# Performance work log

Hardware: AMD Instinct MI355X
Metric: run time of the kernel (lower is better)

The kernel has to match this reference:

```python
import jax, jax.numpy as jnp
import numpy as np

N, E, DIN, HID, G, L = 50000, 200000, 128, 128, 64, 6
H1, H2 = 8, 4
EPS_LN, EPS_BN = 1e-5, 1e-5


def setup_inputs() -> dict:
    key = jax.random.key(0)
    ks = iter(jax.random.split(key, 32))
    def nrm(shape, scale=0.05):
        return jax.random.normal(next(ks), shape, dtype=jnp.float32) * scale
    z = lambda *s: jnp.zeros(s, jnp.float32)
    o = lambda *s: jnp.ones(s, jnp.float32)
    return {
        'x': jax.random.normal(next(ks), (N, DIN), dtype=jnp.float32),
        'edge_index': jax.random.randint(next(ks), (2, E), 0, N),
        'batch': jnp.sort(jax.random.randint(next(ks), (N,), 0, G)),
        'W1': nrm((DIN, H1 * HID)), 'a_src1': nrm((H1, HID)), 'a_dst1': nrm((H1, HID)), 'b1': z(H1 * HID),
        'W2': nrm((H1 * HID, H2 * HID)), 'a_src2': nrm((H2, HID)), 'a_dst2': nrm((H2, HID)), 'b2': z(H2 * HID),
        'W3': nrm((H2 * HID, HID)), 'b3': z(HID),
        'wq': nrm((L, HID, HID)), 'bq': z(L, HID), 'wk': nrm((L, HID, HID)), 'bk': z(L, HID),
        'wv': nrm((L, HID, HID)), 'bv': z(L, HID), 'wo': nrm((L, HID, HID)), 'bo': z(L, HID),
        'ln1g': o(L, HID), 'ln1b': z(L, HID), 'ln2g': o(L, HID), 'ln2b': z(L, HID),
        'wf1': nrm((L, HID, 4 * HID)), 'bf1': z(L, 4 * HID), 'wf2': nrm((L, 4 * HID, HID)), 'bf2': z(L, HID),
        'bn1_g': o(2 * HID), 'bn1_b': z(2 * HID),
        'fc1_w': nrm((2 * HID, HID // 2)), 'fc1_b': z(HID // 2),
        'bn2_g': o(HID // 2), 'bn2_b': z(HID // 2),
        'fc2_w': nrm((HID // 2, 2)), 'fc2_b': z(2),
    }


def _ln(x, g, b):
    mu = x.mean(-1, keepdims=True)
    v = ((x - mu) ** 2).mean(-1, keepdims=True)
    return (x - mu) * jax.lax.rsqrt(v + EPS_LN) * g + b


def _gat(x, src, dst, W, a_s, a_d, b, heads):
    # PyG GATConv: message src -> dst, segment softmax over incoming edges per dst.
    h = (x @ W).reshape(x.shape[0], heads, -1)           # [N, H, C]
    e = jax.nn.leaky_relu((h * a_s).sum(-1)[src] + (h * a_d).sum(-1)[dst], 0.2)  # [E, H]
    m = jax.ops.segment_max(e, dst, num_segments=N)
    ex = jnp.exp(e - jnp.where(jnp.isfinite(m), m, 0.0)[dst])
    s = jax.ops.segment_sum(ex, dst, num_segments=N)
    alpha = ex / (s[dst] + 1e-16)
    out = jax.ops.segment_sum(alpha[:, :, None] * h[src], dst, num_segments=N)
    return out.reshape(N, -1) + b


def _forward(x, edge_index, batch, W1, a_src1, a_dst1, b1, W2, a_src2, a_dst2, b2, W3, b3,
             wq, bq, wk, bk, wv, bv, wo, bo, ln1g, ln1b, ln2g, ln2b, wf1, bf1, wf2, bf2,
             bn1_g, bn1_b, fc1_w, fc1_b, bn2_g, bn2_b, fc2_w, fc2_b):
    loop = jnp.arange(N, dtype=edge_index.dtype)
    src = jnp.concatenate([edge_index[0], loop])          # add self-loops (PyG default)
    dst = jnp.concatenate([edge_index[1], loop])
    h = jax.nn.elu(_gat(x, src, dst, W1, a_src1, a_dst1, b1, H1))
    h = jax.nn.elu(_gat(h, src, dst, W2, a_src2, a_dst2, b2, H2))
    # GCNConv with symmetric normalization (self-loops already included)
    deg = jax.ops.segment_sum(jnp.ones(src.shape, h.dtype), dst, num_segments=N)
    dinv = jnp.where(deg > 0, jax.lax.rsqrt(jnp.maximum(deg, 1e-12)), 0.0)
    norm = dinv[src] * dinv[dst]
    h = jax.nn.elu(jax.ops.segment_sum(norm[:, None] * (h @ W3)[src], dst, num_segments=N) + b3)
    # TransformerEncoder over seq_len=1 (h3.unsqueeze(1)): softmax over one key == 1,
    # so MHA output == Wo @ (Wv h + bv) + bo exactly; q/k have no effect on the output.
    for l in range(L):
        sa = (h @ wv[l] + bv[l]) @ wo[l] + bo[l]
        h = _ln(h + sa, ln1g[l], ln1b[l])
        ff = jax.nn.gelu(h @ wf1[l] + bf1[l], approximate=False) @ wf2[l] + bf2[l]
        h = _ln(h + ff, ln2g[l], ln2b[l])
    # global mean / max pool over graphs
    cnt = jax.ops.segment_sum(jnp.ones((N,), h.dtype), batch, num_segments=G)
    hm = jax.ops.segment_sum(h, batch, num_segments=G) / jnp.maximum(cnt, 1.0)[:, None]
    hx = jax.ops.segment_max(h, batch, num_segments=G)
    hx = jnp.where(jnp.isfinite(hx), hx, 0.0)
    hc = jnp.concatenate([hm, hx], axis=1)                # [G, 2*HID]
    bn_s = 1.0 / np.sqrt(1.0 + EPS_BN)                    # eval BN: running stats (0, 1)
    hc = hc * bn_s * bn1_g + bn1_b
    hc = jax.nn.elu(hc @ fc1_w + fc1_b)
    hc = hc * bn_s * bn2_g + bn2_b
    return hc @ fc2_w + fc2_b                             # [G, 2]


def reference(x, edge_index, batch, W1, a_src1, a_dst1, b1, W2, a_src2, a_dst2, b2, W3, b3,
              wq, bq, wk, bk, wv, bv, wo, bo, ln1g, ln1b, ln2g, ln2b, wf1, bf1, wf2, bf2,
              bn1_g, bn1_b, fc1_w, fc1_b, bn2_g, bn2_b, fc2_w, fc2_b):
    return _forward(x, edge_index, batch, W1, a_src1, a_dst1, b1, W2, a_src2, a_dst2, b2, W3, b3,
                    wq, bq, wk, bk, wv, bv, wo, bo, ln1g, ln1b, ln2g, ln2b, wf1, bf1, wf2, bf2,
                    bn1_g, bn1_b, fc1_w, fc1_b, bn2_g, bn2_b, fc2_w, fc2_b)
```

## Files before the change

kernel.cpp:

```cpp
#include <hip/hip_runtime.h>
#include <hip/hip_bf16.h>
#include <math.h>

#define NN 50000
#define EE 200000
#define ET 250000
#define GG 64
#define LL 6

using short8 = __attribute__((ext_vector_type(8))) short;
using f32x4  = __attribute__((ext_vector_type(4))) float;
typedef unsigned short ushortT;

__device__ __forceinline__ float elu1(float x) { return x > 0.f ? x : expm1f(x); }
__device__ __forceinline__ float gelu_exact(float x) {
    return 0.5f * x * (1.f + erff(x * 0.70710678118654752440f));
}
__device__ __forceinline__ short f2bf(float f) {
    __hip_bfloat16 h = __float2bfloat16(f);
    return *reinterpret_cast<short*>(&h);
}
__device__ __forceinline__ float bf2f(ushortT u) {
    return __uint_as_float(((unsigned)u) << 16);
}

__global__ void count_deg_kernel(const int* __restrict__ ei, int* __restrict__ deg) {
    int e = blockIdx.x * 256 + threadIdx.x;
    if (e >= ET) return;
    int dst = (e < EE) ? ei[EE + e] : (e - EE);
    atomicAdd(&deg[dst], 1);
}

__global__ void scan_kernel(const int* __restrict__ deg, int* __restrict__ row_ptr, int n) {
    __shared__ int s[1024];
    int tid = threadIdx.x;
    const int per = (n + 1023) / 1024;
    int lo = tid * per, hi = min(lo + per, n);
    int sum = 0;
    for (int i = lo; i < hi; i++) sum += deg[i];
    s[tid] = sum;
    __syncthreads();
    for (int off = 1; off < 1024; off <<= 1) {
        int t = (tid >= off) ? s[tid - off] : 0;
        __syncthreads();
        s[tid] += t;
        __syncthreads();
    }
    int run = s[tid] - sum;
    for (int i = lo; i < hi; i++) { row_ptr[i] = run; run += deg[i]; }
    if (tid == 1023) row_ptr[n] = s[1023];
}

__global__ void fill_csr_kernel(const int* __restrict__ ei, const int* __restrict__ row_ptr,
                                int* __restrict__ cursor, int* __restrict__ edge_src) {
    int e = blockIdx.x * 256 + threadIdx.x;
    if (e >= ET) return;
    int src, dst;
    if (e < EE) { src = ei[e]; dst = ei[EE + e]; }
    else        { src = e - EE; dst = e - EE; }
    int pos = atomicAdd(&cursor[dst], 1);
    edge_src[row_ptr[dst] + pos] = src;
}

__global__ void dinv_kernel(const int* __restrict__ row_ptr, float* __restrict__ dinv) {
    int n = blockIdx.x * 256 + threadIdx.x;
    if (n >= NN) return;
    int d = row_ptr[n + 1] - row_ptr[n];
    dinv[n] = (d > 0) ? rsqrtf((float)d) : 0.f;
}

__global__ void wvwo_kernel(const float* __restrict__ wv, const float* __restrict__ wo,
                            const float* __restrict__ bv, const float* __restrict__ bo,
                            float* __restrict__ Wvo, float* __restrict__ bvo) {
    int l = blockIdx.y;
    const float* Wv = wv + l * 16384;
    const float* Wo = wo + l * 16384;
    int tid = blockIdx.x * 256 + threadIdx.x;
    if (tid < 16384) {
        int r = tid >> 7, c = tid & 127;
        float s = 0.f;
        for (int k = 0; k < 128; k++) s += Wv[r * 128 + k] * Wo[k * 128 + c];
        Wvo[l * 16384 + tid] = s;
    }
    if (blockIdx.x == 0 && threadIdx.x < 128) {
        int c = threadIdx.x;
        float s = bo[l * 128 + c];
        for (int k = 0; k < 128; k++) s += bv[l * 128 + k] * Wo[k * 128 + c];
        bvo[l * 128 + c] = s;
    }
}

__global__ void bprep_kernel(const float* __restrict__ B, short* __restrict__ Bp,
                             int K, int N, int ldb, long srcStride) {
    int layer = blockIdx.y;
    const float* Bsrc = B + srcStride * layer;
    short* Bd = Bp + (size_t)K * N * layer;
    int total = (K >> 5) * (N >> 4) * 64;
    int tid = blockIdx.x * 256 + threadIdx.x;
    if (tid >= total) return;
    int l = tid & 63;
    int rest = tid >> 6;
    int kbc = K >> 5;
    int kb = rest % kbc;
    int c16 = rest / kbc;
    int n = c16 * 16 + (l & 15);
    int kbase = kb * 32 + (l >> 4) * 8;
    short v[8];
#pragma unroll
    for (int j = 0; j < 8; j++) v[j] = f2bf(Bsrc[(size_t)(kbase + j) * ldb + n]);
    *(uint4*)(Bd + (size_t)tid * 8) = *(uint4*)v;
}

__global__ void cast_bf16_kernel(const float* __restrict__ in, short* __restrict__ out, int n4) {
    int i = blockIdx.x * 256 + threadIdx.x;
    if (i >= n4) return;
    float4 v = *(const float4*)(in + (size_t)i * 4);
    short s[4] = { f2bf(v.x), f2bf(v.y), f2bf(v.z), f2bf(v.w) };
    *(uint2*)(out + (size_t)i * 4) = *(uint2*)s;
}

template <int EPI, bool BIAS, bool OUTBF16, int NSPLIT, int KBC>
__global__ __launch_bounds__(256) void gemm_bf16_kernel(
    const short* __restrict__ A, const short* __restrict__ Bp,
    const float* __restrict__ bias, void* __restrict__ Cv,
    const float* __restrict__ a_s, const float* __restrict__ a_d,
    float* __restrict__ as_out, float* __restrict__ ad_out, int asH,
    const ushortT* __restrict__ Rres, const float* __restrict__ lng,
    const float* __restrict__ lnb, float* __restrict__ Qout,
    __hip_bfloat16* __restrict__ Qbout,
    int M, int K, int Nc) {
    __shared__ short Bs[(KBC > 0) ? KBC * 4096 : 8192];
    int t = threadIdx.x;
    int w = t >> 6, l = t & 63;
    int ln = l & 15, lq = l >> 4;
    int MBceil = (M + 63) >> 6;
    int bx = blockIdx.x;
    int xcd = bx & 7, idx = bx >> 3;
    int t2 = idx % NSPLIT;
    int mb = (idx / NSPLIT) * 8 + xcd;
    if (mb >= MBceil) return;
    int bm = mb * 64 + w * 16;
    int arow = bm + ln;
    bool aok = arow < M;
    int rowb = bm + lq * 4;
    const short* Ap = A + (size_t)arow * K + lq * 8;

    f32x4 acc[8];
#pragma unroll
    for (int j = 0; j < 8; j++) acc[j] = (f32x4){0.f, 0.f, 0.f, 0.f};

    if constexpr (KBC > 0) {
        {
            const uint4* src = (const uint4*)(Bp + (size_t)t2 * KBC * 4096);
            uint4* dst = (uint4*)Bs;
#pragma unroll
            for (int i = 0; i < KBC * 2; i++)
                dst[i * 256 + t] = src[i * 256 + t];
        }
        short8 af[KBC];
#pragma unroll
        for (int kb = 0; kb < KBC; kb++)
            af[kb] = aok ? *(const short8*)(Ap + kb * 32) : (short8){0,0,0,0,0,0,0,0};
        __syncthreads();
#pragma unroll
        for (int kb = 0; kb < KBC; kb++)
#pragma unroll
            for (int ct = 0; ct < 8; ct++) {
                short8 bfr = *(const short8*)(Bs + ((ct * KBC + kb) * 64 + l) * 8);
                acc[ct] = __builtin_amdgcn_mfma_f32_16x16x32_bf16(af[kb], bfr, acc[ct], 0, 0, 0);
            }
    } else {
        int kbc = K >> 5;
        int sct = t >> 5, spart = t & 31;
        auto stage = [&](int buf, int kb) {
            const uint4* src = (const uint4*)(Bp + ((size_t)(t2 * 8 + sct) * kbc + kb) * 512);
            uint4* dst = (uint4*)(Bs + buf * 4096 + sct * 512);
            dst[spart * 2]     = src[spart * 2];
            dst[spart * 2 + 1] = src[spart * 2 + 1];
        };
        stage(0, 0);
        __syncthreads();
        for (int kb = 0; kb < kbc; kb++) {
            if (kb + 1 < kbc) stage((kb + 1) & 1, kb + 1);
            short8 af = aok ? *(const short8*)(Ap + kb * 32) : (short8){0,0,0,0,0,0,0,0};
            const short* bsb = Bs + (kb & 1) * 4096;
#pragma unroll
            for (int ct = 0; ct < 8; ct++) {
                short8 bfr = *(const short8*)(bsb + (ct * 64 + l) * 8);
                acc[ct] = __builtin_amdgcn_mfma_f32_16x16x32_bf16(af, bfr, acc[ct], 0, 0, 0);
            }
            __syncthreads();
        }
    }

    if (EPI == 2) {
        const float* asv = a_s + t2 * 128;
        const float* adv = a_d + t2 * 128;
#pragma unroll
        for (int reg = 0; reg < 4; reg++) {
            float vs = 0.f, vd = 0.f;
#pragma unroll
            for (int ct = 0; ct < 8; ct++) {
                int colL = ct * 16 + ln;
                float av = acc[ct][reg];
                vs += av * asv[colL];
                vd += av * adv[colL];
            }
            vs += __shfl_xor(vs, 1); vs += __shfl_xor(vs, 2);
            vs += __shfl_xor(vs, 4); vs += __shfl_xor(vs, 8);
            vd += __shfl_xor(vd, 1); vd += __shfl_xor(vd, 2);
            vd += __shfl_xor(vd, 4); vd += __shfl_xor(vd, 8);
            int row = rowb + reg;
            if (ln == 0 && row < M) {
                as_out[(size_t)row * asH + t2] = vs;
                ad_out[(size_t)row * asH + t2] = vd;
            }
        }
    }
    if (EPI == 3) {
        float v[8][4];
#pragma unroll
        for (int ct = 0; ct < 8; ct++) {
            int col = ct * 16 + ln;
            float bv_ = bias[col];
#pragma unroll
            for (int reg = 0; reg < 4; reg++) {
                int row = rowb + reg;
                float r = (row < M) ? bf2f(Rres[(size_t)row * 128 + col]) : 0.f;
                v[ct][reg] = acc[ct][reg] + bv_ + r;
            }
        }
#pragma unroll
        for (int reg = 0; reg < 4; reg++) {
            float s = 0.f;
#pragma unroll
            for (int ct = 0; ct < 8; ct++) s += v[ct][reg];
            s += __shfl_xor(s, 1); s += __shfl_xor(s, 2);
            s += __shfl_xor(s, 4); s += __shfl_xor(s, 8);
            float mean = s * (1.f / 128.f);
            float s2 = 0.f;
#pragma unroll
            for (int ct = 0; ct < 8; ct++) { float d = v[ct][reg] - mean; s2 += d * d; }
            s2 += __shfl_xor(s2, 1); s2 += __shfl_xor(s2, 2);
            s2 += __shfl_xor(s2, 4); s2 += __shfl_xor(s2, 8);
            float rstd = rsqrtf(s2 * (1.f / 128.f) + 1e-5f);
            int row = rowb + reg;
            if (row < M) {
#pragma unroll
                for (int ct = 0; ct < 8; ct++) {
                    int col = ct * 16 + ln;
                    float o = (v[ct][reg] - mean) * rstd * lng[col] + lnb[col];
                    Qbout[(size_t)row * 128 + col] = __float2bfloat16(o);
                    if (Qout) Qout[(size_t)row * 128 + col] = o;
                }
            }
        }
    }
    if (EPI == 0 || EPI == 1 || EPI == 2) {
#pragma unroll
        for (int ct = 0; ct < 8; ct++) {
            int col = t2 * 128 + ct * 16 + ln;
            float bv_ = BIAS ? bias[col] : 0.f;
#pragma unroll
            for (int reg = 0; reg < 4; reg++) {
                int row = rowb + reg;
                if (row < M) {
                    float v = acc[ct][reg] + bv_;
                    if (EPI == 1) v = gelu_exact(v);
                    if (OUTBF16)
                        ((__hip_bfloat16*)Cv)[(size_t)row * Nc + col] = __float2bfloat16(v);
                    else
                        ((float*)Cv)[(size_t)row * Nc + col] = v;
                }
            }
        }
    }
}

template <int H>
__global__ __launch_bounds__(256) void gat_agg_fused_kernel(
    const ushortT* __restrict__ hpre, const float* __restrict__ as_,
    const float* __restrict__ ad_, const float* __restrict__ bias,
    const int* __restrict__ row_ptr, const int* __restrict__ edge_src,
    __hip_bfloat16* __restrict__ out, int n_nodes) {
    const int CPT = H;
    int node = blockIdx.x * 2 + (threadIdx.x >> 7);
    if (node >= n_nodes) return;
    int tt = threadIdx.x & 127;
    int c0 = tt * CPT;
    int hb = c0 >> 7;
    int start = row_ptr[node];
    int deg = row_ptr[node + 1] - start;
    float adn = ad_[(size_t)node * H + hb];
    float m = -1e30f, S = 0.f;
    float acc[CPT];
#pragma unroll
    for (int c = 0; c < CPT; c++) acc[c] = 0.f;
    for (int j = 0; j < deg; j++) {
        int s = edge_src[start + j];
        float e = as_[(size_t)s * H + hb] + adn;
        e = e > 0.f ? e : 0.2f * e;
        float mn = fmaxf(m, e);
        float sc = expf(m - mn);
        float wj = expf(e - mn);
        S = S * sc + wj;
        const ushortT* hp = hpre + (size_t)s * (H * 128) + c0;
        float hv[CPT];
        if (CPT == 8) {
            uint4 u = *(const uint4*)hp;
            hv[0] = bf2f((ushortT)(u.x & 0xffff)); hv[1] = bf2f((ushortT)(u.x >> 16));
            hv[2] = bf2f((ushortT)(u.y & 0xffff)); hv[3] = bf2f((ushortT)(u.y >> 16));
            hv[4] = bf2f((ushortT)(u.z & 0xffff)); hv[5] = bf2f((ushortT)(u.z >> 16));
            hv[6] = bf2f((ushortT)(u.w & 0xffff)); hv[7] = bf2f((ushortT)(u.w >> 16));
        } else {
            uint2 u = *(const uint2*)hp;
            hv[0] = bf2f((ushortT)(u.x & 0xffff)); hv[1] = bf2f((ushortT)(u.x >> 16));
            hv[2] = bf2f((ushortT)(u.y & 0xffff)); hv[3] = bf2f((ushortT)(u.y >> 16));
        }
#pragma unroll
        for (int c = 0; c < CPT; c++) acc[c] = acc[c] * sc + wj * hv[c];
        m = mn;
    }
    float inv = 1.f / (S + 1e-16f);
#pragma unroll
    for (int c = 0; c < CPT; c++)
        out[(size_t)node * (H * 128) + c0 + c] =
            __float2bfloat16(elu1(acc[c] * inv + bias[c0 + c]));
}

__global__ __launch_bounds__(256) void gcn_agg_kernel(
    const ushortT* __restrict__ hp, const float* __restrict__ dinv,
    const float* __restrict__ b3, const int* __restrict__ row_ptr,
    const int* __restrict__ edge_src,
    __hip_bfloat16* __restrict__ outb, int n_nodes) {
    int node = blockIdx.x * 2 + (threadIdx.x >> 7);
    int c = threadIdx.x & 127;
    if (node >= n_nodes) return;
    int start = row_ptr[node];
    int deg = row_ptr[node + 1] - start;
    float dn = dinv[node];
    float acc = 0.f;
    for (int j = 0; j < deg; j++) {
        int s = edge_src[start + j];
        acc += dinv[s] * dn * bf2f(hp[(size_t)s * 128 + c]);
    }
    outb[(size_t)node * 128 + c] = __float2bfloat16(elu1(acc + b3[c]));
}

__global__ void pool1_kernel(const float* __restrict__ Q, const int* __restrict__ batch,
                             float* __restrict__ psum, float* __restrict__ pmax, int n_nodes) {
    int g = blockIdx.x, seg = blockIdx.y;
    int c = threadIdx.x;
    int lo, hi;
    {
        int l = 0, h = n_nodes;
        while (l < h) { int mid = (l + h) >> 1; if (batch[mid] < g) l = mid + 1; else h = mid; }
        lo = l;
        l = lo; h = n_nodes;
        while (l < h) { int mid = (l + h) >> 1; if (batch[mid] < g + 1) l = mid + 1; else h = mid; }
        hi = l;
    }
    int len = hi - lo;
    int a = lo + (int)((long)len * seg / 8);
    int b = lo + (int)((long)len * (seg + 1) / 8);
    float s = 0.f, mx = -INFINITY;
    for (int n = a; n < b; n++) {
        float v = Q[(size_t)n * 128 + c];
        s += v;
        mx = fmaxf(mx, v);
    }
    psum[(g * 8 + seg) * 128 + c] = s;
    pmax[(g * 8 + seg) * 128 + c] = mx;
}

__global__ void pool2_kernel(const float* __restrict__ psum, const float* __restrict__ pmax,
                             const int* __restrict__ batch,
                             const float* __restrict__ bn1g, const float* __restrict__ bn1b,
                             float* __restrict__ hc, int n_nodes) {
    int g = blockIdx.x;
    int c = threadIdx.x;
    int lo, hi;
    {
        int l = 0, h = n_nodes;
        while (l < h) { int mid = (l + h) >> 1; if (batch[mid] < g) l = mid + 1; else h = mid; }
        lo = l;
        l = lo; h = n_nodes;
        while (l < h) { int mid = (l + h) >> 1; if (batch[mid] < g + 1) l = mid + 1; else h = mid; }
        hi = l;
    }
    int cnt = hi - lo;
    float s = 0.f, mx = -INFINITY;
    for (int seg = 0; seg < 8; seg++) {
        s += psum[(g * 8 + seg) * 128 + c];
        mx = fmaxf(mx, pmax[(g * 8 + seg) * 128 + c]);
    }
    float hm = s / fmaxf((float)cnt, 1.f);
    float hx = (cnt > 0 && isfinite(mx)) ? mx : 0.f;
    const float bn_s = 0.99999500003749968f;
    hc[g * 256 + c]       = hm * bn_s * bn1g[c] + bn1b[c];
    hc[g * 256 + 128 + c] = hx * bn_s * bn1g[128 + c] + bn1b[128 + c];
}

__global__ void head_kernel(const float* __restrict__ hc,
                            const float* __restrict__ fc1w, const float* __restrict__ fc1b,
                            const float* __restrict__ bn2g, const float* __restrict__ bn2b,
                            const float* __restrict__ fc2w, const float* __restrict__ fc2b,
                            float* __restrict__ out) {
    int g = blockIdx.x;
    int j = threadIdx.x;
    const float bn_s = 0.99999500003749968f;
    float acc = fc1b[j];
    for (int i = 0; i < 256; i++) acc += hc[g * 256 + i] * fc1w[i * 64 + j];
    acc = elu1(acc);
    acc = acc * bn_s * bn2g[j] + bn2b[j];
    __shared__ float sv[64];
    sv[j] = acc;
    __syncthreads();
    if (j < 2) {
        float o = fc2b[j];
        for (int i = 0; i < 64; i++) o += sv[i] * fc2w[i * 2 + j];
        out[g * 2 + j] = o;
    }
}

extern "C" void kernel_launch(void* const* d_in, const int* in_sizes, int n_in,
                              void* d_out, int out_size, void* d_ws, size_t ws_size,
                              hipStream_t stream) {
    const float* x    = (const float*)d_in[0];
    const int*   ei   = (const int*)d_in[1];
    const int*   batch= (const int*)d_in[2];
    const float* W1   = (const float*)d_in[3];
    const float* as1  = (const float*)d_in[4];
    const float* ad1  = (const float*)d_in[5];
    const float* b1   = (const float*)d_in[6];
    const float* W2   = (const float*)d_in[7];
    const float* as2  = (const float*)d_in[8];
    const float* ad2  = (const float*)d_in[9];
    const float* b2   = (const float*)d_in[10];
    const float* W3   = (const float*)d_in[11];
    const float* b3   = (const float*)d_in[12];
    const float* wv   = (const float*)d_in[17];
    const float* bv   = (const float*)d_in[18];
    const float* wo   = (const float*)d_in[19];
    const float* bo   = (const float*)d_in[20];
    const float* ln1g = (const float*)d_in[21];
    const float* ln1b = (const float*)d_in[22];
    const float* ln2g = (const float*)d_in[23];
    const float* ln2b = (const float*)d_in[24];
    const float* wf1  = (const float*)d_in[25];
    const float* bf1  = (const float*)d_in[26];
    const float* wf2  = (const float*)d_in[27];
    const float* bf2  = (const float*)d_in[28];
    const float* bn1g = (const float*)d_in[29];
    const float* bn1b = (const float*)d_in[30];
    const float* fc1w = (const float*)d_in[31];
    const float* fc1b = (const float*)d_in[32];
    const float* bn2g = (const float*)d_in[33];
    const float* bn2b = (const float*)d_in[34];
    const float* fc2w = (const float*)d_in[35];
    const float* fc2b = (const float*)d_in[36];
    float* out = (float*)d_out;

    char* wsb = (char*)d_ws;
    short* xb    = (short*)wsb;
    short* h1pre = (short*)(wsb + 12800000);
    short* h2pre = (short*)(wsb + 12800000);
    short* h3pre = (short*)(wsb + 12800000);
    short* FFb   = (short*)(wsb + 25600000);
    short* bh1   = (short*)(wsb + 115200000);
    short* bh2   = (short*)(wsb + 115200000);
    float* fQ    = (float*)(wsb + 128000000);
    short* Qb    = (short*)(wsb + 153600000);
    char* tail = wsb + 217600000;
    short* W1p  = (short*)tail;  tail += 262144;
    short* W2p  = (short*)tail;  tail += 1048576;
    short* W3p  = (short*)tail;  tail += 131072;
    short* Wvop = (short*)tail;  tail += 196608;
    short* wf1p = (short*)tail;  tail += 786432;
    short* wf2p = (short*)tail;  tail += 786432;
    float* Wvo  = (float*)tail;  tail += 393216;
    float* bvo  = (float*)tail;  tail += 3072;
    float* fAS  = (float*)tail;  tail += 1600000;
    float* fAD  = (float*)tail;  tail += 1600000;
    float* fDv  = (float*)tail;  tail += 200000;
    float* psum = (float*)tail;  tail += 262144;
    float* pmax = (float*)tail;  tail += 262144;
    float* fHC  = (float*)tail;  tail += 65536;
    int* iDeg   = (int*)tail;    tail += 200000;
    int* iRP    = (int*)tail;    tail += 200004;
    int* iCur   = (int*)tail;    tail += 200000;
    int* iES    = (int*)tail;    tail += 1000000;

    hipMemsetAsync(iDeg, 0, NN * sizeof(int), stream);
    hipMemsetAsync(iCur, 0, NN * sizeof(int), stream);

    count_deg_kernel<<<(ET + 255) / 256, 256, 0, stream>>>(ei, iDeg);
    scan_kernel<<<1, 1024, 0, stream>>>(iDeg, iRP, NN);
    fill_csr_kernel<<<(ET + 255) / 256, 256, 0, stream>>>(ei, iRP, iCur, iES);
    dinv_kernel<<<(NN + 255) / 256, 256, 0, stream>>>(iRP, fDv);

    wvwo_kernel<<<dim3(64, 6), 256, 0, stream>>>(wv, wo, bv, bo, Wvo, bvo);
    auto bprep = [&](const float* B, short* Bp, int K, int N, int ldb, long sStride, int layers) {
        int total = (K >> 5) * (N >> 4) * 64;
        dim3 grid((total + 255) / 256, layers);
        bprep_kernel<<<grid, 256, 0, stream>>>(B, Bp, K, N, ldb, sStride);
    };
    bprep(W1, W1p, 128, 1024, 1024, 0, 1);
    bprep(W2, W2p, 1024, 512, 512, 0, 1);
    bprep(W3, W3p, 512, 128, 128, 0, 1);
    bprep(Wvo, Wvop, 128, 128, 128, 16384, 6);
    bprep(wf1, wf1p, 128, 512, 512, 65536, 6);
    bprep(wf2, wf2p, 512, 128, 128, 65536, 6);
    cast_bf16_kernel<<<(NN * 128 / 4 + 255) / 256, 256, 0, stream>>>(x, xb, NN * 128 / 4);

    const int MB64 = (NN + 63) / 64;
    const int MBp = ((MB64 + 7) / 8) * 8;

    gemm_bf16_kernel<2, false, true, 8, 4><<<MBp * 8, 256, 0, stream>>>(
        xb, W1p, nullptr, h1pre, as1, ad1, fAS, fAD, 8,
        nullptr, nullptr, nullptr, nullptr, nullptr, NN, 128, 1024);
    gat_agg_fused_kernel<8><<<(NN + 1) / 2, 256, 0, stream>>>(
        (const ushortT*)h1pre, fAS, fAD, b1, iRP, iES, (__hip_bfloat16*)bh1, NN);
    gemm_bf16_kernel<2, false, true, 4, 0><<<MBp * 4, 256, 0, stream>>>(
        bh1, W2p, nullptr, h2pre, as2, ad2, fAS, fAD, 4,
        nullptr, nullptr, nullptr, nullptr, nullptr, NN, 1024, 512);
    gat_agg_fused_kernel<4><<<(NN + 1) / 2, 256, 0, stream>>>(
        (const ushortT*)h2pre, fAS, fAD, b2, iRP, iES, (__hip_bfloat16*)bh2, NN);
    gemm_bf16_kernel<0, false, true, 1, 0><<<MBp, 256, 0, stream>>>(
        bh2, W3p, nullptr, h3pre, nullptr, nullptr, nullptr, nullptr, 0,
        nullptr, nullptr, nullptr, nullptr, nullptr, NN, 512, 128);
    gcn_agg_kernel<<<(NN + 1) / 2, 256, 0, stream>>>(
        (const ushortT*)h3pre, fDv, b3, iRP, iES, (__hip_bfloat16*)Qb, NN);
    for (int l = 0; l < LL; l++) {
        gemm_bf16_kernel<3, true, false, 1, 4><<<MBp, 256, 0, stream>>>(
            Qb, Wvop + l * 16384, bvo + l * 128, nullptr, nullptr, nullptr, nullptr, nullptr, 0,
            (const ushortT*)Qb, ln1g + l * 128, ln1b + l * 128, nullptr, (__hip_bfloat16*)Qb,
            NN, 128, 128);
        gemm_bf16_kernel<1, true, true, 4, 4><<<MBp * 4, 256, 0, stream>>>(
            Qb, wf1p + l * 65536, bf1 + l * 512, FFb, nullptr, nullptr, nullptr, nullptr, 0,
            nullptr, nullptr, nullptr, nullptr, nullptr, NN, 128, 512);
        gemm_bf16_kernel<3, true, false, 1, 0><<<MBp, 256, 0, stream>>>(
            FFb, wf2p + l * 65536, bf2 + l * 128, nullptr, nullptr, nullptr, nullptr, nullptr, 0,
            (const ushortT*)Qb, ln2g + l * 128, ln2b + l * 128,
            (l == LL - 1) ? fQ : nullptr, (__hip_bfloat16*)Qb, NN, 512, 128);
    }
    pool1_kernel<<<dim3(GG, 8), 128, 0, stream>>>(fQ, batch, psum, pmax, NN);
    pool2_kernel<<<GG, 128, 0, stream>>>(psum, pmax, batch, bn1g, bn1b, fHC, NN);
    head_kernel<<<GG, 64, 0, stream>>>(fHC, fc1w, fc1b, bn2g, bn2b, fc2w, fc2b, out);
}
```

Before: 1.335 ms.

## Add multi-row-tile GEMM variant and precompute GAT attention weights in separate kernel

The GEMM kernel gains an RT template parameter so each wave computes several 16-row tiles against the same shared-memory B fragment. This raises data reuse per B load for the K-looped GEMMs (W2, W3, wf2) but increases register pressure. Separately, the GAT softmax is split out: a new alpha_kernel computes per-edge exp weights and the inverse sum per node/head. The aggregation kernel then only does a weighted sum, dropping the online-softmax rescaling and the redundant exp work across 128 threads, at the cost of an extra launch and an alpha buffer round trip through memory.

New measurement: 1.429 ms. 1.07x slower.

```diff
diff --git a/kernel.cpp b/kernel.cpp
--- a/kernel.cpp
+++ b/kernel.cpp
@@ -119,80 +119,15 @@
     *(uint2*)(out + (size_t)i * 4) = *(uint2*)s;
 }
 
-template <int EPI, bool BIAS, bool OUTBF16, int NSPLIT, int KBC>
-__global__ __launch_bounds__(256) void gemm_bf16_kernel(
-    const short* __restrict__ A, const short* __restrict__ Bp,
+template <int EPI, bool BIAS, bool OUTBF16>
+__device__ __forceinline__ void epi_store(
+    int t2, f32x4 (&acc)[8], int M, int Nc, int rowb, int ln,
     const float* __restrict__ bias, void* __restrict__ Cv,
     const float* __restrict__ a_s, const float* __restrict__ a_d,
     float* __restrict__ as_out, float* __restrict__ ad_out, int asH,
     const ushortT* __restrict__ Rres, const float* __restrict__ lng,
     const float* __restrict__ lnb, float* __restrict__ Qout,
-    __hip_bfloat16* __restrict__ Qbout,
-    int M, int K, int Nc) {
-    __shared__ short Bs[(KBC > 0) ? KBC * 4096 : 8192];
-    int t = threadIdx.x;
-    int w = t >> 6, l = t & 63;
-    int ln = l & 15, lq = l >> 4;
-    int MBceil = (M + 63) >> 6;
-    int bx = blockIdx.x;
-    int xcd = bx & 7, idx = bx >> 3;
-    int t2 = idx % NSPLIT;
-    int mb = (idx / NSPLIT) * 8 + xcd;
-    if (mb >= MBceil) return;
-    int bm = mb * 64 + w * 16;
-    int arow = bm + ln;
-    bool aok = arow < M;
-    int rowb = bm + lq * 4;
-    const short* Ap = A + (size_t)arow * K + lq * 8;
-
-    f32x4 acc[8];
-#pragma unroll
-    for (int j = 0; j < 8; j++) acc[j] = (f32x4){0.f, 0.f, 0.f, 0.f};
-
-    if constexpr (KBC > 0) {
-        {
-            const uint4* src = (const uint4*)(Bp + (size_t)t2 * KBC * 4096);
-            uint4* dst = (uint4*)Bs;
-#pragma unroll
-            for (int i = 0; i < KBC * 2; i++)
-                dst[i * 256 + t] = src[i * 256 + t];
-        }
-        short8 af[KBC];
-#pragma unroll
-        for (int kb = 0; kb < KBC; kb++)
-            af[kb] = aok ? *(const short8*)(Ap + kb * 32) : (short8){0,0,0,0,0,0,0,0};
-        __syncthreads();
-#pragma unroll
-        for (int kb = 0; kb < KBC; kb++)
-#pragma unroll
-            for (int ct = 0; ct < 8; ct++) {
-                short8 bfr = *(const short8*)(Bs + ((ct * KBC + kb) * 64 + l) * 8);
-                acc[ct] = __builtin_amdgcn_mfma_f32_16x16x32_bf16(af[kb], bfr, acc[ct], 0, 0, 0);
-            }
-    } else {
-        int kbc = K >> 5;
-        int sct = t >> 5, spart = t & 31;
-        auto stage = [&](int buf, int kb) {
-            const uint4* src = (const uint4*)(Bp + ((size_t)(t2 * 8 + sct) * kbc + kb) * 512);
-            uint4* dst = (uint4*)(Bs + buf * 4096 + sct * 512);
-            dst[spart * 2]     = src[spart * 2];
-            dst[spart * 2 + 1] = src[spart * 2 + 1];
-        };
-        stage(0, 0);
-        __syncthreads();
-        for (int kb = 0; kb < kbc; kb++) {
-            if (kb + 1 < kbc) stage((kb + 1) & 1, kb + 1);
-            short8 af = aok ? *(const short8*)(Ap + kb * 32) : (short8){0,0,0,0,0,0,0,0};
-            const short* bsb = Bs + (kb & 1) * 4096;
-#pragma unroll
-            for (int ct = 0; ct < 8; ct++) {
-                short8 bfr = *(const short8*)(bsb + (ct * 64 + l) * 8);
-                acc[ct] = __builtin_amdgcn_mfma_f32_16x16x32_bf16(af, bfr, acc[ct], 0, 0, 0);
-            }
-            __syncthreads();
-        }
-    }
-
+    __hip_bfloat16* __restrict__ Qbout) {
     if (EPI == 2) {
         const float* asv = a_s + t2 * 128;
         const float* adv = a_d + t2 * 128;
@@ -277,10 +212,140 @@
     }
 }
 
+template <int EPI, bool BIAS, bool OUTBF16, int NSPLIT, int KBC, int RT>
+__global__ __launch_bounds__(256) void gemm_bf16_kernel(
+    const short* __restrict__ A, const short* __restrict__ Bp,
+    const float* __restrict__ bias, void* __restrict__ Cv,
+    const float* __restrict__ a_s, const float* __restrict__ a_d,
+    float* __restrict__ as_out, float* __restrict__ ad_out, int asH,
+    const ushortT* __restrict__ Rres, const float* __restrict__ lng,
+    const float* __restrict__ lnb, float* __restrict__ Qout,
+    __hip_bfloat16* __restrict__ Qbout,
+    int M, int K, int Nc) {
+    __shared__ short Bs[(KBC > 0) ? KBC * 4096 : 8192];
+    int t = threadIdx.x;
+    int w = t >> 6, l = t & 63;
+    int ln = l & 15, lq = l >> 4;
+    const int ROWS = 64 * RT;
+    int MBceil = (M + ROWS - 1) / ROWS;
+    int bx = blockIdx.x;
+    int xcd = bx & 7, idx = bx >> 3;
+    int t2 = idx % NSPLIT;
+    int mb = (idx / NSPLIT) * 8 + xcd;
+    if (mb >= MBceil) return;
+    int wbase = mb * ROWS + w * 16;
+
+    bool aok[RT];
+    const short* Ap[RT];
+#pragma unroll
+    for (int rt = 0; rt < RT; rt++) {
+        int r = wbase + rt * 64 + ln;
+        aok[rt] = r < M;
+        Ap[rt] = A + (size_t)r * K + lq * 8;
+    }
+
+    f32x4 acc[RT][8];
+#pragma unroll
+    for (int rt = 0; rt < RT; rt++)
+#pragma unroll
+        for (int j = 0; j < 8; j++) acc[rt][j] = (f32x4){0.f, 0.f, 0.f, 0.f};
+
+    if constexpr (KBC > 0) {
+        {
+            const uint4* src = (const uint4*)(Bp + (size_t)t2 * KBC * 4096);
+            uint4* dst = (uint4*)Bs;
+#pragma unroll
+            for (int i = 0; i < KBC * 2; i++)
+                dst[i * 256 + t] = src[i * 256 + t];
+        }
+        short8 af[RT][KBC];
+#pragma unroll
+        for (int rt = 0; rt < RT; rt++)
+#pragma unroll
+            for (int kb = 0; kb < KBC; kb++)
+                af[rt][kb] = aok[rt] ? *(const short8*)(Ap[rt] + kb * 32)
+                                     : (short8){0,0,0,0,0,0,0,0};
+        __syncthreads();
+#pragma unroll
+        for (int kb = 0; kb < KBC; kb++)
+#pragma unroll
+            for (int ct = 0; ct < 8; ct++) {
+                short8 bfr = *(const short8*)(Bs + ((ct * KBC + kb) * 64 + l) * 8);
+#pragma unroll
+                for (int rt = 0; rt < RT; rt++)
+                    acc[rt][ct] = __builtin_amdgcn_mfma_f32_16x16x32_bf16(af[rt][kb], bfr, acc[rt][ct], 0, 0, 0);
+            }
+    } else {
+        int kbc = K >> 5;
+        int sct = t >> 5, spart = t & 31;
+        auto stage = [&](int buf, int kb) {
+            const uint4* src = (const uint4*)(Bp + ((size_t)(t2 * 8 + sct) * kbc + kb) * 512);
+            uint4* dst = (uint4*)(Bs + buf * 4096 + sct * 512);
+            dst[spart * 2]     = src[spart * 2];
+            dst[spart * 2 + 1] = src[spart * 2 + 1];
+        };
+        stage(0, 0);
+        __syncthreads();
+        for (int kb = 0; kb < kbc; kb++) {
+            if (kb + 1 < kbc) stage((kb + 1) & 1, kb + 1);
+            short8 af[RT];
+#pragma unroll
+            for (int rt = 0; rt < RT; rt++)
+                af[rt] = aok[rt] ? *(const short8*)(Ap[rt] + kb * 32)
+                                 : (short8){0,0,0,0,0,0,0,0};
+            const short* bsb = Bs + (kb & 1) * 4096;
+#pragma unroll
+            for (int ct = 0; ct < 8; ct++) {
+                short8 bfr = *(const short8*)(bsb + (ct * 64 + l) * 8);
+#pragma unroll
+                for (int rt = 0; rt < RT; rt++)
+                    acc[rt][ct] = __builtin_amdgcn_mfma_f32_16x16x32_bf16(af[rt], bfr, acc[rt][ct], 0, 0, 0);
+            }
+            __syncthreads();
+        }
+    }
+
+#pragma unroll
+    for (int rt = 0; rt < RT; rt++) {
+        int rowb = wbase + rt * 64 + lq * 4;
+        epi_store<EPI, BIAS, OUTBF16>(t2, acc[rt], M, Nc, rowb, ln, bias, Cv,
+            a_s, a_d, as_out, ad_out, asH, Rres, lng, lnb, Qout, Qbout);
+    }
+}
+
+template <int H>
+__global__ __launch_bounds__(256) void alpha_kernel(
+    const float* __restrict__ as_, const float* __restrict__ ad_,
+    const int* __restrict__ row_ptr, const int* __restrict__ edge_src,
+    float* __restrict__ alpha, float* __restrict__ Sinv, int n_nodes) {
+    int idx = blockIdx.x * 256 + threadIdx.x;
+    if (idx >= n_nodes * H) return;
+    int n = idx / H, h = idx % H;
+    int start = row_ptr[n], deg = row_ptr[n + 1] - start;
+    float adn = ad_[(size_t)n * H + h];
+    float m = -1e30f;
+    for (int j = 0; j < deg; j++) {
+        int s = edge_src[start + j];
+        float e = as_[(size_t)s * H + h] + adn;
+        e = e > 0.f ? e : 0.2f * e;
+        m = fmaxf(m, e);
+    }
+    float S = 0.f;
+    for (int j = 0; j < deg; j++) {
+        int s = edge_src[start + j];
+        float e = as_[(size_t)s * H + h] + adn;
+        e = e > 0.f ? e : 0.2f * e;
+        float wv = expf(e - m);
+        S += wv;
+        alpha[(size_t)(start + j) * H + h] = wv;
+    }
+    Sinv[(size_t)n * H + h] = 1.f / (S + 1e-16f);
+}
+
 template <int H>
 __global__ __launch_bounds__(256) void gat_agg_fused_kernel(
-    const ushortT* __restrict__ hpre, const float* __restrict__ as_,
-    const float* __restrict__ ad_, const float* __restrict__ bias,
+    const ushortT* __restrict__ hpre, const float* __restrict__ alpha,
+    const float* __restrict__ Sinv, const float* __restrict__ bias,
     const int* __restrict__ row_ptr, const int* __restrict__ edge_src,
     __hip_bfloat16* __restrict__ out, int n_nodes) {
     const int CPT = H;
@@ -291,19 +356,13 @@
     int hb = c0 >> 7;
     int start = row_ptr[node];
     int deg = row_ptr[node + 1] - start;
-    float adn = ad_[(size_t)node * H + hb];
-    float m = -1e30f, S = 0.f;
+    float inv = Sinv[(size_t)node * H + hb];
     float acc[CPT];
 #pragma unroll
     for (int c = 0; c < CPT; c++) acc[c] = 0.f;
     for (int j = 0; j < deg; j++) {
         int s = edge_src[start + j];
-        float e = as_[(size_t)s * H + hb] + adn;
-        e = e > 0.f ? e : 0.2f * e;
-        float mn = fmaxf(m, e);
-        float sc = expf(m - mn);
-        float wj = expf(e - mn);
-        S = S * sc + wj;
+        float wv = alpha[(size_t)(start + j) * H + hb];
         const ushortT* hp = hpre + (size_t)s * (H * 128) + c0;
         float hv[CPT];
         if (CPT == 8) {
@@ -318,10 +377,8 @@
             hv[2] = bf2f((ushortT)(u.y & 0xffff)); hv[3] = bf2f((ushortT)(u.y >> 16));
         }
 #pragma unroll
-        for (int c = 0; c < CPT; c++) acc[c] = acc[c] * sc + wj * hv[c];
-        m = mn;
-    }
-    float inv = 1.f / (S + 1e-16f);
+        for (int c = 0; c < CPT; c++) acc[c] += wv * hv[c];
+    }
 #pragma unroll
     for (int c = 0; c < CPT; c++)
         out[(size_t)node * (H * 128) + c0 + c] =
@@ -463,6 +520,8 @@
 
     char* wsb = (char*)d_ws;
     short* xb    = (short*)wsb;
+    float* alpha = (float*)wsb;
+    float* Sinv  = (float*)(wsb + 8000000);
     short* h1pre = (short*)(wsb + 12800000);
     short* h2pre = (short*)(wsb + 12800000);
     short* h3pre = (short*)(wsb + 12800000);
@@ -513,33 +572,37 @@
     bprep(wf2, wf2p, 512, 128, 128, 65536, 6);
     cast_bf16_kernel<<<(NN * 128 / 4 + 255) / 256, 256, 0, stream>>>(x, xb, NN * 128 / 4);
 
-    const int MB64 = (NN + 63) / 64;
-    const int MBp = ((MB64 + 7) / 8) * 8;
-
-    gemm_bf16_kernel<2, false, true, 8, 4><<<MBp * 8, 256, 0, stream>>>(
+    const int MB64p  = (((NN + 63) / 64 + 7) / 8) * 8;
+    const int MB128p = (((NN + 127) / 128 + 7) / 8) * 8;
+
+    gemm_bf16_kernel<2, false, true, 8, 4, 1><<<MB64p * 8, 256, 0, stream>>>(
         xb, W1p, nullptr, h1pre, as1, ad1, fAS, fAD, 8,
         nullptr, nullptr, nullptr, nullptr, nullptr, NN, 128, 1024);
+    alpha_kernel<8><<<(NN * 8 + 255) / 256, 256, 0, stream>>>(
+        fAS, fAD, iRP, iES, alpha, Sinv, NN);
     gat_agg_fused_kernel<8><<<(NN + 1) / 2, 256, 0, stream>>>(
-        (const ushortT*)h1pre, fAS, fAD, b1, iRP, iES, (__hip_bfloat16*)bh1, NN);
-    gemm_bf16_kernel<2, false, true, 4, 0><<<MBp * 4, 256, 0, stream>>>(
+        (const ushortT*)h1pre, alpha, Sinv, b1, iRP, iES, (__hip_bfloat16*)bh1, NN);
+    gemm_bf16_kernel<2, false, true, 4, 0, 2><<<MB128p * 4, 256, 0, stream>>>(
         bh1, W2p, nullptr, h2pre, as2, ad2, fAS, fAD, 4,
         nullptr, nullptr, nullptr, nullptr, nullptr, NN, 1024, 512);
+    alpha_kernel<4><<<(NN * 4 + 255) / 256, 256, 0, stream>>>(
+        fAS, fAD, iRP, iES, alpha, Sinv, NN);
     gat_agg_fused_kernel<4><<<(NN + 1) / 2, 256, 0, stream>>>(
-        (const ushortT*)h2pre, fAS, fAD, b2, iRP, iES, (__hip_bfloat16*)bh2, NN);
-    gemm_bf16_kernel<0, false, true, 1, 0><<<MBp, 256, 0, stream>>>(
+        (const ushortT*)h2pre, alpha, Sinv, b2, iRP, iES, (__hip_bfloat16*)bh2, NN);
+    gemm_bf16_kernel<0, false, true, 1, 0, 2><<<MB128p, 256, 0, stream>>>(
         bh2, W3p, nullptr, h3pre, nullptr, nullptr, nullptr, nullptr, 0,
         nullptr, nullptr, nullptr, nullptr, nullptr, NN, 512, 128);
     gcn_agg_kernel<<<(NN + 1) / 2, 256, 0, stream>>>(
         (const ushortT*)h3pre, fDv, b3, iRP, iES, (__hip_bfloat16*)Qb, NN);
     for (int l = 0; l < LL; l++) {
-        gemm_bf16_kernel<3, true, false, 1, 4><<<MBp, 256, 0, stream>>>(
+        gemm_bf16_kernel<3, true, false, 1, 4, 1><<<MB64p, 256, 0, stream>>>(
             Qb, Wvop + l * 16384, bvo + l * 128, nullptr, nullptr, nullptr, nullptr, nullptr, 0,
             (const ushortT*)Qb, ln1g + l * 128, ln1b + l * 128, nullptr, (__hip_bfloat16*)Qb,
             NN, 128, 128);
-        gemm_bf16_kernel<1, true, true, 4, 4><<<MBp * 4, 256, 0, stream>>>(
+        gemm_bf16_kernel<1, true, true, 4, 4, 1><<<MB64p * 4, 256, 0, stream>>>(
             Qb, wf1p + l * 65536, bf1 + l * 512, FFb, nullptr, nullptr, nullptr, nullptr, 0,
             nullptr, nullptr, nullptr, nullptr, nullptr, NN, 128, 512);
-        gemm_bf16_kernel<3, true, false, 1, 0><<<MBp, 256, 0, stream>>>(
+        gemm_bf16_kernel<3, true, false, 1, 0, 2><<<MB128p, 256, 0, stream>>>(
             FFb, wf2p + l * 65536, bf2 + l * 128, nullptr, nullptr, nullptr, nullptr, nullptr, 0,
             (const ushortT*)Qb, ln2g + l * 128, ln2b + l * 128,
             (l == LL - 1) ? fQ : nullptr, (__hip_bfloat16*)Qb, NN, 512, 128);
```

## Fuse transformer FFN up/down GEMMs with residual LayerNorm into one kernel

Applied to the files above, without the earlier changes.

Replaces the two per-layer FFN GEMM launches (128->512 with GELU, then 512->128 with residual+LayerNorm) with one kernel. Each wave keeps its 16-row activation tile in registers and computes the 512-wide hidden layer in four 128-column chunks. Each chunk goes through a small per-wave LDS buffer and is accumulated straight into the down-projection, so the bf16 intermediate FFb is never written to or read from global memory. In exchange, weights are read directly from global memory without LDS staging, each block does more serial MFMA work, and the residual read and in-place write of Qb across blocks depend on rows being disjoint.

Result: slower. 1.411 ms (+5.6%).

```diff
diff --git a/kernel.cpp b/kernel.cpp
--- a/kernel.cpp
+++ b/kernel.cpp
@@ -117,6 +117,99 @@
     float4 v = *(const float4*)(in + (size_t)i * 4);
     short s[4] = { f2bf(v.x), f2bf(v.y), f2bf(v.z), f2bf(v.w) };
     *(uint2*)(out + (size_t)i * 4) = *(uint2*)s;
+}
+
+template <int EPI, bool BIAS, bool OUTBF16>
+__device__ __forceinline__ void epi_store(
+    int t2, f32x4 (&acc)[8], int M, int Nc, int rowb, int ln,
+    const float* __restrict__ bias, void* __restrict__ Cv,
+    const float* __restrict__ a_s, const float* __restrict__ a_d,
+    float* __restrict__ as_out, float* __restrict__ ad_out, int asH,
+    const ushortT* __restrict__ Rres, const float* __restrict__ lng,
+    const float* __restrict__ lnb, float* __restrict__ Qout,
+    __hip_bfloat16* __restrict__ Qbout) {
+    if (EPI == 2) {
+        const float* asv = a_s + t2 * 128;
+        const float* adv = a_d + t2 * 128;
+#pragma unroll
+        for (int reg = 0; reg < 4; reg++) {
+            float vs = 0.f, vd = 0.f;
+#pragma unroll
+            for (int ct = 0; ct < 8; ct++) {
+                int colL = ct * 16 + ln;
+                float av = acc[ct][reg];
+                vs += av * asv[colL];
+                vd += av * adv[colL];
+            }
+            vs += __shfl_xor(vs, 1); vs += __shfl_xor(vs, 2);
+            vs += __shfl_xor(vs, 4); vs += __shfl_xor(vs, 8);
+            vd += __shfl_xor(vd, 1); vd += __shfl_xor(vd, 2);
+            vd += __shfl_xor(vd, 4); vd += __shfl_xor(vd, 8);
+            int row = rowb + reg;
+            if (ln == 0 && row < M) {
+                as_out[(size_t)row * asH + t2] = vs;
+                ad_out[(size_t)row * asH + t2] = vd;
+            }
+        }
+    }
+    if (EPI == 3) {
+        float v[8][4];
+#pragma unroll
+        for (int ct = 0; ct < 8; ct++) {
+            int col = ct * 16 + ln;
+            float bv_ = bias[col];
+#pragma unroll
+            for (int reg = 0; reg < 4; reg++) {
+                int row = rowb + reg;
+                float r = (row < M) ? bf2f(Rres[(size_t)row * 128 + col]) : 0.f;
+                v[ct][reg] = acc[ct][reg] + bv_ + r;
+            }
+        }
+#pragma unroll
+        for (int reg = 0; reg < 4; reg++) {
+            float s = 0.f;
+#pragma unroll
+            for (int ct = 0; ct < 8; ct++) s += v[ct][reg];
+            s += __shfl_xor(s, 1); s += __shfl_xor(s, 2);
+            s += __shfl_xor(s, 4); s += __shfl_xor(s, 8);
+            float mean = s * (1.f / 128.f);
+            float s2 = 0.f;
+#pragma unroll
+            for (int ct = 0; ct < 8; ct++) { float d = v[ct][reg] - mean; s2 += d * d; }
+            s2 += __shfl_xor(s2, 1); s2 += __shfl_xor(s2, 2);
+            s2 += __shfl_xor(s2, 4); s2 += __shfl_xor(s2, 8);
+            float rstd = rsqrtf(s2 * (1.f / 128.f) + 1e-5f);
+            int row = rowb + reg;
+            if (row < M) {
+#pragma unroll
+                for (int ct = 0; ct < 8; ct++) {
+                    int col = ct * 16 + ln;
+                    float o = (v[ct][reg] - mean) * rstd * lng[col] + lnb[col];
+                    Qbout[(size_t)row * 128 + col] = __float2bfloat16(o);
+                    if (Qout) Qout[(size_t)row * 128 + col] = o;
+                }
+            }
+        }
+    }
+    if (EPI == 0 || EPI == 1 || EPI == 2) {
+#pragma unroll
+        for (int ct = 0; ct < 8; ct++) {
+            int col = t2 * 128 + ct * 16 + ln;
+            float bv_ = BIAS ? bias[col] : 0.f;
+#pragma unroll
+            for (int reg = 0; reg < 4; reg++) {
+                int row = rowb + reg;
+                if (row < M) {
+                    float v = acc[ct][reg] + bv_;
+                    if (EPI == 1) v = gelu_exact(v);
+                    if (OUTBF16)
+                        ((__hip_bfloat16*)Cv)[(size_t)row * Nc + col] = __float2bfloat16(v);
+                    else
+                        ((float*)Cv)[(size_t)row * Nc + col] = v;
+                }
+            }
+        }
+    }
 }
 
 template <int EPI, bool BIAS, bool OUTBF16, int NSPLIT, int KBC>
@@ -193,85 +286,99 @@
         }
     }
 
-    if (EPI == 2) {
-        const float* asv = a_s + t2 * 128;
-        const float* adv = a_d + t2 * 128;
+    epi_store<EPI, BIAS, OUTBF16>(t2, acc, M, Nc, rowb, ln, bias, Cv,
+        a_s, a_d, as_out, ad_out, asH, Rres, lng, lnb, Qout, Qbout);
+}
+
+__global__ __launch_bounds__(256) void ffn_fused_kernel(
+    const short* __restrict__ Qb, const short* __restrict__ wf1p_l,
+    const float* __restrict__ bf1_l, const short* __restrict__ wf2p_l,
+    const float* __restrict__ bf2_l, const float* __restrict__ lng,
+    const float* __restrict__ lnb, float* __restrict__ Qout,
+    int M) {
+    __shared__ short Hs[4][16][130];
+    int t = threadIdx.x;
+    int w = t >> 6, l = t & 63;
+    int ln = l & 15, lq = l >> 4;
+    int wbase = blockIdx.x * 64 + w * 16;
+    int arow = wbase + ln;
+    bool aok = arow < M;
+    const short* Ap = Qb + (size_t)arow * 128 + lq * 8;
+    short (*Hw)[130] = Hs[w];
+
+    short8 af[4];
+#pragma unroll
+    for (int kb = 0; kb < 4; kb++)
+        af[kb] = aok ? *(const short8*)(Ap + kb * 32) : (short8){0,0,0,0,0,0,0,0};
+
+    f32x4 out[8];
+#pragma unroll
+    for (int j = 0; j < 8; j++) out[j] = (f32x4){0.f, 0.f, 0.f, 0.f};
+
+#pragma unroll
+    for (int c = 0; c < 4; c++) {
+#pragma unroll
+        for (int ct = 0; ct < 8; ct++) {
+            f32x4 h4 = (f32x4){0.f, 0.f, 0.f, 0.f};
+#pragma unroll
+            for (int kb = 0; kb < 4; kb++) {
+                short8 bfr = *(const short8*)(wf1p_l + (((c * 8 + ct) * 4 + kb) * 64 + l) * 8);
+                h4 = __builtin_amdgcn_mfma_f32_16x16x32_bf16(af[kb], bfr, h4, 0, 0, 0);
+            }
+            int col = ct * 16 + ln;
+            float bb = bf1_l[c * 128 + col];
+#pragma unroll
+            for (int reg = 0; reg < 4; reg++)
+                Hw[lq * 4 + reg][col] = f2bf(gelu_exact(h4[reg] + bb));
+        }
+        short8 hf[4];
+#pragma unroll
+        for (int kb2 = 0; kb2 < 4; kb2++)
+            hf[kb2] = *(const short8*)&Hw[ln][kb2 * 32 + lq * 8];
+#pragma unroll
+        for (int ct = 0; ct < 8; ct++)
+#pragma unroll
+            for (int kb2 = 0; kb2 < 4; kb2++) {
+                short8 bfr = *(const short8*)(wf2p_l + ((ct * 16 + c * 4 + kb2) * 64 + l) * 8);
+                out[ct] = __builtin_amdgcn_mfma_f32_16x16x32_bf16(hf[kb2], bfr, out[ct], 0, 0, 0);
+            }
+    }
+
+    int rowb = wbase + lq * 4;
+    float v[8][4];
+#pragma unroll
+    for (int ct = 0; ct < 8; ct++) {
+        int col = ct * 16 + ln;
+        float bv_ = bf2_l[col];
 #pragma unroll
         for (int reg = 0; reg < 4; reg++) {
-            float vs = 0.f, vd = 0.f;
+            int row = rowb + reg;
+            float r = (row < M) ? bf2f(((const ushortT*)Qb)[(size_t)row * 128 + col]) : 0.f;
+            v[ct][reg] = out[ct][reg] + bv_ + r;
+        }
+    }
+#pragma unroll
+    for (int reg = 0; reg < 4; reg++) {
+        float s = 0.f;
+#pragma unroll
+        for (int ct = 0; ct < 8; ct++) s += v[ct][reg];
+        s += __shfl_xor(s, 1); s += __shfl_xor(s, 2);
+        s += __shfl_xor(s, 4); s += __shfl_xor(s, 8);
+        float mean = s * (1.f / 128.f);
+        float s2 = 0.f;
+#pragma unroll
+        for (int ct = 0; ct < 8; ct++) { float d = v[ct][reg] - mean; s2 += d * d; }
+        s2 += __shfl_xor(s2, 1); s2 += __shfl_xor(s2, 2);
+        s2 += __shfl_xor(s2, 4); s2 += __shfl_xor(s2, 8);
+        float rstd = rsqrtf(s2 * (1.f / 128.f) + 1e-5f);
+        int row = rowb + reg;
+        if (row < M) {
 #pragma unroll
             for (int ct = 0; ct < 8; ct++) {
-                int colL = ct * 16 + ln;
-                float av = acc[ct][reg];
-                vs += av * asv[colL];
-                vd += av * adv[colL];
-            }
-            vs += __shfl_xor(vs, 1); vs += __shfl_xor(vs, 2);
-            vs += __shfl_xor(vs, 4); vs += __shfl_xor(vs, 8);
-            vd += __shfl_xor(vd, 1); vd += __shfl_xor(vd, 2);
-            vd += __shfl_xor(vd, 4); vd += __shfl_xor(vd, 8);
-            int row = rowb + reg;
-            if (ln == 0 && row < M) {
-                as_out[(size_t)row * asH + t2] = vs;
-                ad_out[(size_t)row * asH + t2] = vd;
-            }
-        }
-    }
-    if (EPI == 3) {
-        float v[8][4];
-#pragma unroll
-        for (int ct = 0; ct < 8; ct++) {
-            int col = ct * 16 + ln;
-            float bv_ = bias[col];
-#pragma unroll
-            for (int reg = 0; reg < 4; reg++) {
-                int row = rowb + reg;
-                float r = (row < M) ? bf2f(Rres[(size_t)row * 128 + col]) : 0.f;
-                v[ct][reg] = acc[ct][reg] + bv_ + r;
-            }
-        }
-#pragma unroll
-        for (int reg = 0; reg < 4; reg++) {
-            float s = 0.f;
-#pragma unroll
-            for (int ct = 0; ct < 8; ct++) s += v[ct][reg];
-            s += __shfl_xor(s, 1); s += __shfl_xor(s, 2);
-            s += __shfl_xor(s, 4); s += __shfl_xor(s, 8);
-            float mean = s * (1.f / 128.f);
-            float s2 = 0.f;
-#pragma unroll
-            for (int ct = 0; ct < 8; ct++) { float d = v[ct][reg] - mean; s2 += d * d; }
-            s2 += __shfl_xor(s2, 1); s2 += __shfl_xor(s2, 2);
-            s2 += __shfl_xor(s2, 4); s2 += __shfl_xor(s2, 8);
-            float rstd = rsqrtf(s2 * (1.f / 128.f) + 1e-5f);
-            int row = rowb + reg;
-            if (row < M) {
-#pragma unroll
-                for (int ct = 0; ct < 8; ct++) {
-                    int col = ct * 16 + ln;
-                    float o = (v[ct][reg] - mean) * rstd * lng[col] + lnb[col];
-                    Qbout[(size_t)row * 128 + col] = __float2bfloat16(o);
-                    if (Qout) Qout[(size_t)row * 128 + col] = o;
-                }
-            }
-        }
-    }
-    if (EPI == 0 || EPI == 1 || EPI == 2) {
-#pragma unroll
-        for (int ct = 0; ct < 8; ct++) {
-            int col = t2 * 128 + ct * 16 + ln;
-            float bv_ = BIAS ? bias[col] : 0.f;
-#pragma unroll
-            for (int reg = 0; reg < 4; reg++) {
-                int row = rowb + reg;
-                if (row < M) {
-                    float v = acc[ct][reg] + bv_;
-                    if (EPI == 1) v = gelu_exact(v);
-                    if (OUTBF16)
-                        ((__hip_bfloat16*)Cv)[(size_t)row * Nc + col] = __float2bfloat16(v);
-                    else
-                        ((float*)Cv)[(size_t)row * Nc + col] = v;
-                }
+                int col = ct * 16 + ln;
+                float o = (v[ct][reg] - mean) * rstd * lng[col] + lnb[col];
+                ((__hip_bfloat16*)Qb)[(size_t)row * 128 + col] = __float2bfloat16(o);
+                if (Qout) Qout[(size_t)row * 128 + col] = o;
             }
         }
     }
@@ -466,7 +573,6 @@
     short* h1pre = (short*)(wsb + 12800000);
     short* h2pre = (short*)(wsb + 12800000);
     short* h3pre = (short*)(wsb + 12800000);
-    short* FFb   = (short*)(wsb + 25600000);
     short* bh1   = (short*)(wsb + 115200000);
     short* bh2   = (short*)(wsb + 115200000);
     float* fQ    = (float*)(wsb + 128000000);
@@ -513,36 +619,32 @@
     bprep(wf2, wf2p, 512, 128, 128, 65536, 6);
     cast_bf16_kernel<<<(NN * 128 / 4 + 255) / 256, 256, 0, stream>>>(x, xb, NN * 128 / 4);
 
-    const int MB64 = (NN + 63) / 64;
-    const int MBp = ((MB64 + 7) / 8) * 8;
-
-    gemm_bf16_kernel<2, false, true, 8, 4><<<MBp * 8, 256, 0, stream>>>(
+    const int MB64  = (NN + 63) / 64;
+    const int MB64p = ((MB64 + 7) / 8) * 8;
+
+    gemm_bf16_kernel<2, false, true, 8, 4><<<MB64p * 8, 256, 0, stream>>>(
         xb, W1p, nullptr, h1pre, as1, ad1, fAS, fAD, 8,
         nullptr, nullptr, nullptr, nullptr, nullptr, NN, 128, 1024);
     gat_agg_fused_kernel<8><<<(NN + 1) / 2, 256, 0, stream>>>(
         (const ushortT*)h1pre, fAS, fAD, b1, iRP, iES, (__hip_bfloat16*)bh1, NN);
-    gemm_bf16_kernel<2, false, true, 4, 0><<<MBp * 4, 256, 0, stream>>>(
+    gemm_bf16_kernel<2, false, true, 4, 0><<<MB64p * 4, 256, 0, stream>>>(
         bh1, W2p, nullptr, h2pre, as2, ad2, fAS, fAD, 4,
         nullptr, nullptr, nullptr, nullptr, nullptr, NN, 1024, 512);
     gat_agg_fused_kernel<4><<<(NN + 1) / 2, 256, 0, stream>>>(
         (const ushortT*)h2pre, fAS, fAD, b2, iRP, iES, (__hip_bfloat16*)bh2, NN);
-    gemm_bf16_kernel<0, false, true, 1, 0><<<MBp, 256, 0, stream>>>(
+    gemm_bf16_kernel<0, false, true, 1, 0><<<MB64p, 256, 0, stream>>>(
         bh2, W3p, nullptr, h3pre, nullptr, nullptr, nullptr, nullptr, 0,
         nullptr, nullptr, nullptr, nullptr, nullptr, NN, 512, 128);
     gcn_agg_kernel<<<(NN + 1) / 2, 256, 0, stream>>>(
         (const ushortT*)h3pre, fDv, b3, iRP, iES, (__hip_bfloat16*)Qb, NN);
     for (int l = 0; l < LL; l++) {
-        gemm_bf16_kernel<3, true, false, 1, 4><<<MBp, 256, 0, stream>>>(
+        gemm_bf16_kernel<3, true, false, 1, 4><<<MB64p, 256, 0, stream>>>(
             Qb, Wvop + l * 16384, bvo + l * 128, nullptr, nullptr, nullptr, nullptr, nullptr, 0,
             (const ushortT*)Qb, ln1g + l * 128, ln1b + l * 128, nullptr, (__hip_bfloat16*)Qb,
             NN, 128, 128);
-        gemm_bf16_kernel<1, true, true, 4, 4><<<MBp * 4, 256, 0, stream>>>(
-            Qb, wf1p + l * 65536, bf1 + l * 512, FFb, nullptr, nullptr, nullptr, nullptr, 0,
-            nullptr, nullptr, nullptr, nullptr, nullptr, NN, 128, 512);
-        gemm_bf16_kernel<3, true, false, 1, 0><<<MBp, 256, 0, stream>>>(
-            FFb, wf2p + l * 65536, bf2 + l * 128, nullptr, nullptr, nullptr, nullptr, nullptr, 0,
-            (const ushortT*)Qb, ln2g + l * 128, ln2b + l * 128,
-            (l == LL - 1) ? fQ : nullptr, (__hip_bfloat16*)Qb, NN, 512, 128);
+        ffn_fused_kernel<<<MB64, 256, 0, stream>>>(
+            Qb, wf1p + l * 65536, bf1 + l * 512, wf2p + l * 65536, bf2 + l * 128,
+            ln2g + l * 128, ln2b + l * 128, (l == LL - 1) ? fQ : nullptr, NN);
     }
     pool1_kernel<<<dim3(GG, 8), 128, 0, stream>>>(fQ, batch, psum, pmax, NN);
     pool2_kernel<<<GG, 128, 0, stream>>>(psum, pmax, batch, bn1g, bn1b, fHC, NN);
```
